# Kernel tuning notes

Hardware: AMD Instinct MI355X
Metric: run time of the kernel (lower is better)

## Reference

```python
import jax, jax.numpy as jnp
import numpy as np
from jax import lax


def setup_inputs() -> dict:
    key = jax.random.key(0)
    B, N, R = 16, 4096, 256
    param = jax.random.normal(key, (B, N, R), dtype=jnp.float32)
    return {"param": param}


def reference(param) -> jnp.ndarray:
    # StiefelHouseholder.forward with is_thin=True (rank != n):
    #   v = tril(param, -1) + eye(n, rank)      -> unit-lower columns v_i
    #   tau_i = 2 / ||v_i||^2
    #   Q = (I - tau_1 v_1 v_1^T) ... (I - tau_R v_R v_R^T) @ I[:, :R]
    B, N, R = param.shape
    eye = jnp.eye(N, R, dtype=param.dtype)                      # [N, R]
    v = jnp.tril(param, k=-1) + eye[None]                       # [B, N, R]
    tau = 2.0 / jnp.sum(v * v, axis=1)                          # [B, R]

    Q0 = jnp.broadcast_to(eye, (B, N, R))                       # start from thin identity

    def body(Q, i):
        vi = v[:, :, i]                                          # [B, N]
        ti = tau[:, i]                                           # [B]
        w = jnp.einsum('bn,bnk->bk', vi, Q)                      # v_i^T Q
        Q = Q - (ti[:, None] * vi)[:, :, None] * w[:, None, :]   # rank-1 update
        return Q, None

    # Apply H_R first (rightmost factor), then H_{R-1}, ..., H_1.
    Q, _ = lax.scan(body, Q0, jnp.arange(R - 1, -1, -1))
    return Q                                                     # thin [B, N, R]
```

## Files before the change

kernel.cpp:

```cpp
#include <hip/hip_runtime.h>
#include <stdint.h>

#define B_ 16
#define N_ 4096
#define R_ 256

typedef short bf16x8 __attribute__((ext_vector_type(8)));
typedef float f32x4 __attribute__((ext_vector_type(4)));
typedef uint32_t u32;


__device__ __forceinline__ u32 pack_split(float x) {
  u32 u = __float_as_uint(x);
  u32 h = u & 0xffff0000u;
  float l = x - __uint_as_float(h);
  return h | (__float_as_uint(l) >> 16);
}

__device__ __forceinline__ void unpack8(const u32* w, bf16x8& hi, bf16x8& lo) {
  union { u32 u[4]; bf16x8 v; } H, L;
#pragma unroll
  for (int i = 0; i < 4; ++i) {
    u32 a = w[2 * i], b = w[2 * i + 1];
    H.u[i] = (a >> 16) | (b & 0xffff0000u);
    L.u[i] = (a & 0xffffu) | (b << 16);
  }
  hi = H.v; lo = L.v;
}

__device__ __forceinline__ void read_frag(const u32* rowbase, int row, int q2,
                                          bf16x8& hi, bf16x8& lo) {
  u32 w[8];
  const int s = row & 7;
  *(uint4*)&w[0] = *(const uint4*)(rowbase + (((q2    ) ^ s) << 2));
  *(uint4*)&w[4] = *(const uint4*)(rowbase + (((q2 + 1) ^ s) << 2));
  unpack8(w, hi, lo);
}

__device__ __forceinline__ f32x4 mm3(bf16x8 ah, bf16x8 al, bf16x8 bh, bf16x8 bl,
                                     f32x4 c) {
  c = __builtin_amdgcn_mfma_f32_16x16x32_bf16(al, bh, c, 0, 0, 0);
  c = __builtin_amdgcn_mfma_f32_16x16x32_bf16(ah, bl, c, 0, 0, 0);
  c = __builtin_amdgcn_mfma_f32_16x16x32_bf16(ah, bh, c, 0, 0, 0);
  return c;
}

__global__ __launch_bounds__(256) void gram_kernel(const float* __restrict__ param,
                                                   float* __restrict__ SP) {
  const int tile = blockIdx.x, chunk = blockIdx.y, b = blockIdx.z;
  const int j0 = (tile == 2) ? 128 : 0;
  const int k0 = (tile == 0) ? 0 : 128;
  const float* __restrict__ P = param + (size_t)b * N_ * R_;

  __shared__ u32 VT[256][32];

  const int t = threadIdx.x;
  const int lane = t & 63, wv = t >> 6;
  const int wr = wv >> 1, wc = wv & 1;
  const int l15 = lane & 15, q = lane >> 4;
  const int bbase = (tile == 1) ? 128 : 0;

  f32x4 acc[4][4];
#pragma unroll
  for (int i = 0; i < 4; ++i)
#pragma unroll
    for (int j = 0; j < 4; ++j) acc[i][j] = (f32x4){0.f, 0.f, 0.f, 0.f};

  const int nb = chunk * 256;
  const int ns = (nb > k0) ? nb : k0;
  const int ne = nb + 256;

  float ld[32];

  const int ct1 = t;
  const int ct0 = t & 127;
  const int gc0 = j0 + ct0;
  const int hb  = t >> 7;

  auto do_load = [&](int n0) {
    if (tile == 1) {
#pragma unroll
      for (int ri = 0; ri < 8; ++ri)
#pragma unroll
        for (int s = 0; s < 4; ++s)
          ld[4 * ri + s] = P[(size_t)(n0 + 4 * ri + s) * R_ + ct1];
    } else {
#pragma unroll
      for (int ri = 0; ri < 4; ++ri)
#pragma unroll
        for (int s = 0; s < 4; ++s)
          ld[4 * ri + s] = P[(size_t)(n0 + 4 * (2 * ri + hb) + s) * R_ + gc0];
    }
  };

  auto do_write = [&](int n0) {
    if (tile == 1) {
#pragma unroll
      for (int ri = 0; ri < 8; ++ri) {
        u32 qw[4];
#pragma unroll
        for (int s = 0; s < 4; ++s) {
          int n = n0 + 4 * ri + s;
          float v = (n == ct1) ? 1.f : ((n > ct1) ? ld[4 * ri + s] : 0.f);
          qw[s] = pack_split(v);
        }
        *(uint4*)&VT[ct1][((ri ^ (ct1 & 7)) << 2)] = *(uint4*)qw;
      }
    } else {
#pragma unroll
      for (int ri = 0; ri < 4; ++ri) {
        int ch = 2 * ri + hb;
        u32 qw[4];
#pragma unroll
        for (int s = 0; s < 4; ++s) {
          int n = n0 + 4 * ch + s;
          float v = (n == gc0) ? 1.f : ((n > gc0) ? ld[4 * ri + s] : 0.f);
          qw[s] = pack_split(v);
        }
        *(uint4*)&VT[ct0][((ch ^ (ct0 & 7)) << 2)] = *(uint4*)qw;
      }
    }
  };

  do_load(ns);
  for (int n0 = ns; n0 < ne; n0 += 32) {
    do_write(n0);
    __syncthreads();
    if (n0 + 32 < ne) do_load(n0 + 32);

    bf16x8 Ah[4], Al[4];
#pragma unroll
    for (int mt = 0; mt < 4; ++mt) {
      int row = 64 * wr + 16 * mt + l15;
      read_frag(&VT[row][0], row, 2 * q, Ah[mt], Al[mt]);
    }
#pragma unroll
    for (int nt = 0; nt < 4; ++nt) {
      int brow = bbase + 64 * wc + 16 * nt + l15;
      bf16x8 bh, bl;
      read_frag(&VT[brow][0], brow, 2 * q, bh, bl);
#pragma unroll
      for (int mt = 0; mt < 4; ++mt)
        acc[mt][nt] = mm3(Ah[mt], Al[mt], bh, bl, acc[mt][nt]);
    }
    __syncthreads();
  }

  float* Sp = SP + (size_t)(chunk * 16 + b) * (R_ * R_);
#pragma unroll
  for (int mt = 0; mt < 4; ++mt)
#pragma unroll
    for (int nt = 0; nt < 4; ++nt) {
      int jj = j0 + 64 * wr + 16 * mt + 4 * q;
      int kk = k0 + 64 * wc + 16 * nt + l15;
#pragma unroll
      for (int r = 0; r < 4; ++r)
        Sp[(size_t)(jj + r) * R_ + kk] = acc[mt][nt][r];
    }
}

__global__ __launch_bounds__(256) void reduce_kernel(float* __restrict__ SP) {
  size_t idx = (size_t)blockIdx.x * 256 + threadIdx.x;
  float4* sp = (float4*)SP;
  float4 a = sp[idx];
#pragma unroll
  for (int c = 1; c < 16; ++c) {
    float4 v = sp[idx + (size_t)c * 262144];
    a.x += v.x; a.y += v.y; a.z += v.z; a.w += v.w;
  }
  sp[idx] = a;
}

#define DPP_ADD(v, ctrl, rmask)                                              \
  v += __int_as_float(__builtin_amdgcn_update_dpp(                           \
      0, __float_as_int(v), ctrl, rmask, 0xf, true))

__global__ __launch_bounds__(1024) void solve_kernel(const float* __restrict__ param,
                                                     const float* __restrict__ S,
                                                     u32* __restrict__ WtP) {
  extern __shared__ float tri[];
  const int t    = threadIdx.x;
  const int lane = t & 63;
  const int wave = t >> 6;
  const int b    = blockIdx.x >> 4;
  const int jg   = blockIdx.x & 15;
  const int k    = jg + 16 * wave;
  const float* __restrict__ Sb = S + (size_t)b * R_ * R_;
  const float* __restrict__ Pb = param + (size_t)b * N_ * R_;

  float4 x = *(const float4*)(Pb + (size_t)k * R_ + 4 * lane);
  {
    int c0 = 4 * lane;
    x.x = (c0     == k) ? 1.f : ((c0     < k) ? x.x : 0.f);
    x.y = (c0 + 1 == k) ? 1.f : ((c0 + 1 < k) ? x.y : 0.f);
    x.z = (c0 + 2 == k) ? 1.f : ((c0 + 2 < k) ? x.z : 0.f);
    x.w = (c0 + 3 == k) ? 1.f : ((c0 + 3 < k) ? x.w : 0.f);
  }

  const float4* S4 = (const float4*)Sb;
#pragma unroll
  for (int m = 0; m < 16; ++m) {
    int idx = t + 1024 * m;
    int r  = idx >> 6;
    int c4 = idx & 63;
    int g  = r >> 2;
    if (c4 >= g) {
      float4 v = S4[idx];
      int rowlen = 256 - 4 * g;
      int addr = 1024 * g - 8 * g * (g - 1) + (r & 3) * rowlen + 4 * (c4 - g);
      *(float4*)&tri[addr] = v;
    }
  }
  __syncthreads();

  float4 w = make_float4(0.f, 0.f, 0.f, 0.f);
  const int k4 = k >> 2;
  int rowlen = 256 - 4 * k4;
  int base   = 1024 * k4 - 8 * k4 * (k4 - 1);

  for (int r4 = k4;; --r4) {
    const float* rb = tri + base + 4 * lane - 4 * r4;
    float4 rA0 = *(const float4*)(rb);
    float4 rA1 = *(const float4*)(rb + rowlen);
    float4 rA2 = *(const float4*)(rb + 2 * rowlen);
    float4 rA3 = *(const float4*)(rb + 3 * rowlen);

    float s0 = fmaf(rA0.x, w.x, fmaf(rA0.y, w.y, fmaf(rA0.z, w.z, rA0.w * w.w)));
    float s1 = fmaf(rA1.x, w.x, fmaf(rA1.y, w.y, fmaf(rA1.z, w.z, rA1.w * w.w)));
    float s2 = fmaf(rA2.x, w.x, fmaf(rA2.y, w.y, fmaf(rA2.z, w.z, rA2.w * w.w)));
    float s3 = fmaf(rA3.x, w.x, fmaf(rA3.y, w.y, fmaf(rA3.z, w.z, rA3.w * w.w)));

    DPP_ADD(s0, 0x111, 0xf); DPP_ADD(s1, 0x111, 0xf);
    DPP_ADD(s2, 0x111, 0xf); DPP_ADD(s3, 0x111, 0xf);
    DPP_ADD(s0, 0x112, 0xf); DPP_ADD(s1, 0x112, 0xf);
    DPP_ADD(s2, 0x112, 0xf); DPP_ADD(s3, 0x112, 0xf);
    DPP_ADD(s0, 0x114, 0xf); DPP_ADD(s1, 0x114, 0xf);
    DPP_ADD(s2, 0x114, 0xf); DPP_ADD(s3, 0x114, 0xf);
    DPP_ADD(s0, 0x118, 0xf); DPP_ADD(s1, 0x118, 0xf);
    DPP_ADD(s2, 0x118, 0xf); DPP_ADD(s3, 0x118, 0xf);
    DPP_ADD(s0, 0x142, 0xa); DPP_ADD(s1, 0x142, 0xa);
    DPP_ADD(s2, 0x142, 0xa); DPP_ADD(s3, 0x142, 0xa);
    DPP_ADD(s0, 0x143, 0xc); DPP_ADD(s1, 0x143, 0xc);
    DPP_ADD(s2, 0x143, 0xc); DPP_ADD(s3, 0x143, 0xc);
    s0 = __int_as_float(__builtin_amdgcn_readlane(__float_as_int(s0), 63));
    s1 = __int_as_float(__builtin_amdgcn_readlane(__float_as_int(s1), 63));
    s2 = __int_as_float(__builtin_amdgcn_readlane(__float_as_int(s2), 63));
    s3 = __int_as_float(__builtin_amdgcn_readlane(__float_as_int(s3), 63));

    float w3 = 2.f * __builtin_amdgcn_rcpf(rA3.w) * (x.w - s3);
    float s2c = fmaf(rA2.w, w3, s2);
    float w2 = 2.f * __builtin_amdgcn_rcpf(rA2.z) * (x.z - s2c);
    float s1c = fmaf(rA1.z, w2, fmaf(rA1.w, w3, s1));
    float w1 = 2.f * __builtin_amdgcn_rcpf(rA1.y) * (x.y - s1c);
    float s0c = fmaf(rA0.y, w1, fmaf(rA0.z, w2, fmaf(rA0.w, w3, s0)));
    float w0 = 2.f * __builtin_amdgcn_rcpf(rA0.x) * (x.x - s0c);
    if (lane == r4) { w.w = w3; w.z = w2; w.y = w1; w.x = w0; }

    if (r4 == 0) break;
    rowlen += 4;
    base   -= 4 * rowlen;
  }

  u32 pw[4] = { pack_split(w.x), pack_split(w.y), pack_split(w.z), pack_split(w.w) };
  *(uint4*)(WtP + ((size_t)b * R_ + k) * R_ + 4 * lane) = *(uint4*)pw;
}

__global__ __launch_bounds__(256) void final_kernel(const float* __restrict__ param,
                                                    const u32* __restrict__ WtP,
                                                    float* __restrict__ Q) {
  const int b  = blockIdx.z;
  const int n0 = blockIdx.x * 128;
  const int k0 = blockIdx.y * 128;
  const float* __restrict__ Pb = param + (size_t)b * N_ * R_;
  const u32* __restrict__ Wb = WtP + (size_t)b * R_ * R_;
  float* __restrict__ Qb = Q + (size_t)b * N_ * R_;

  __shared__ u32 VA[128][32];
  __shared__ u32 WB[128][32];

  const int t = threadIdx.x;
  const int lane = t & 63, wv = t >> 6;
  const int wr = wv >> 1, wc = wv & 1;
  const int l15 = lane & 15, q = lane >> 4;
  const int row8 = t >> 3;
  const int c4 = t & 7;

  f32x4 acc[4][4];
#pragma unroll
  for (int i = 0; i < 4; ++i)
#pragma unroll
    for (int j = 0; j < 4; ++j) acc[i][j] = (f32x4){0.f, 0.f, 0.f, 0.f};

  const int jend = k0 + 128;
  for (int jb = 0; jb < jend; jb += 32) {
#pragma unroll
    for (int pi = 0; pi < 4; ++pi) {
      int row = row8 + 32 * pi;
      int n = n0 + row;
      int gj = jb + 4 * c4;
      float4 v = *(const float4*)&Pb[(size_t)n * R_ + gj];
      u32 qw[4];
      qw[0] = pack_split((n == gj    ) ? 1.f : ((n > gj    ) ? v.x : 0.f));
      qw[1] = pack_split((n == gj + 1) ? 1.f : ((n > gj + 1) ? v.y : 0.f));
      qw[2] = pack_split((n == gj + 2) ? 1.f : ((n > gj + 2) ? v.z : 0.f));
      qw[3] = pack_split((n == gj + 3) ? 1.f : ((n > gj + 3) ? v.w : 0.f));
      *(uint4*)&VA[row][((c4 ^ (row & 7)) << 2)] = *(uint4*)qw;
      uint4 wq = *(const uint4*)&Wb[(size_t)(k0 + row) * R_ + gj];
      *(uint4*)&WB[row][((c4 ^ (row & 7)) << 2)] = wq;
    }
    __syncthreads();

    bf16x8 Ah[4], Al[4];
#pragma unroll
    for (int mt = 0; mt < 4; ++mt) {
      int row = 64 * wr + 16 * mt + l15;
      read_frag(&VA[row][0], row, 2 * q, Ah[mt], Al[mt]);
    }
#pragma unroll
    for (int nt = 0; nt < 4; ++nt) {
      int krow = 64 * wc + 16 * nt + l15;
      bf16x8 bh, bl;
      read_frag(&WB[krow][0], krow, 2 * q, bh, bl);
#pragma unroll
      for (int mt = 0; mt < 4; ++mt)
        acc[mt][nt] = mm3(Ah[mt], Al[mt], bh, bl, acc[mt][nt]);
    }
    __syncthreads();
  }

#pragma unroll
  for (int mt = 0; mt < 4; ++mt)
#pragma unroll
    for (int nt = 0; nt < 4; ++nt) {
      int nrow = n0 + 64 * wr + 16 * mt + 4 * q;
      int kcol = k0 + 64 * wc + 16 * nt + l15;
#pragma unroll
      for (int r = 0; r < 4; ++r) {
        float val = ((nrow + r == kcol) ? 1.f : 0.f) - acc[mt][nt][r];
        Qb[(size_t)(nrow + r) * R_ + kcol] = val;
      }
    }
}

extern "C" void kernel_launch(void* const* d_in, const int* in_sizes, int n_in,
                              void* d_out, int out_size, void* d_ws, size_t ws_size,
                              hipStream_t stream) {
  const float* param = (const float*)d_in[0];
  float* Q  = (float*)d_out;
  float* SP = Q;
  float* S  = Q;
  u32*   WtP = (u32*)d_ws;

  gram_kernel<<<dim3(3, 16, B_), 256, 0, stream>>>(param, SP);
  reduce_kernel<<<dim3(1024), 256, 0, stream>>>(SP);
  solve_kernel<<<dim3(256), 1024, 133120, stream>>>(param, S, WtP);
  final_kernel<<<dim3(32, 2, B_), 256, 0, stream>>>(param, WtP, Q);
}
```

Before: 149.3 us.

## Async global-to-LDS loads and LDS-staged coalesced stores in final kernel

The final kernel now loads the param and W tiles with global_load_lds async copies, issuing the next tile before the MFMA work so loads overlap compute. The raw float V tile is stored in LDS and split into bf16 hi/lo at fragment read time, with the triangular mask applied only to the diagonal blocks. The epilogue stages results through LDS so the Q output is written as coalesced float4 rows instead of scattered scalar stores. The cost is extra barriers and more split work per fragment read, and the epilogue reuses VAf (128x32 floats) with a row stride of 132 for 32 rows, which looks like it overruns the array.

```diff
diff --git a/kernel.cpp b/kernel.cpp
--- a/kernel.cpp
+++ b/kernel.cpp
@@ -37,12 +37,38 @@
   unpack8(w, hi, lo);
 }
 
+__device__ __forceinline__ void read_frag_f(const float* rowbase, int row, int q2,
+                                            bf16x8& hi, bf16x8& lo) {
+  float w[8];
+  const int s = row & 7;
+  *(float4*)&w[0] = *(const float4*)(rowbase + (((q2    ) ^ s) << 2));
+  *(float4*)&w[4] = *(const float4*)(rowbase + (((q2 + 1) ^ s) << 2));
+  union { u32 u[4]; bf16x8 v; } H, L;
+#pragma unroll
+  for (int i = 0; i < 4; ++i) {
+    u32 a = __float_as_uint(w[2 * i]);
+    u32 b = __float_as_uint(w[2 * i + 1]);
+    u32 ah = a & 0xffff0000u, bh = b & 0xffff0000u;
+    float la = w[2 * i]     - __uint_as_float(ah);
+    float lb = w[2 * i + 1] - __uint_as_float(bh);
+    H.u[i] = (a >> 16) | bh;
+    L.u[i] = (__float_as_uint(la) >> 16) | (__float_as_uint(lb) & 0xffff0000u);
+  }
+  hi = H.v; lo = L.v;
+}
+
 __device__ __forceinline__ f32x4 mm3(bf16x8 ah, bf16x8 al, bf16x8 bh, bf16x8 bl,
                                      f32x4 c) {
   c = __builtin_amdgcn_mfma_f32_16x16x32_bf16(al, bh, c, 0, 0, 0);
   c = __builtin_amdgcn_mfma_f32_16x16x32_bf16(ah, bl, c, 0, 0, 0);
   c = __builtin_amdgcn_mfma_f32_16x16x32_bf16(ah, bh, c, 0, 0, 0);
   return c;
+}
+
+typedef __attribute__((address_space(1))) const u32* gas_p;
+typedef __attribute__((address_space(3))) u32* las_p;
+__device__ __forceinline__ void async_cp16(void* lds, const void* g) {
+  __builtin_amdgcn_global_load_lds((gas_p)g, (las_p)lds, 16, 0, 0);
 }
 
 __global__ __launch_bounds__(256) void gram_kernel(const float* __restrict__ param,
@@ -275,15 +301,16 @@
   const u32* __restrict__ Wb = WtP + (size_t)b * R_ * R_;
   float* __restrict__ Qb = Q + (size_t)b * N_ * R_;
 
-  __shared__ u32 VA[128][32];
-  __shared__ u32 WB[128][32];
+  __shared__ float VAf[128][32];
+  __shared__ u32   WBp[128][32];
 
   const int t = threadIdx.x;
   const int lane = t & 63, wv = t >> 6;
   const int wr = wv >> 1, wc = wv & 1;
   const int l15 = lane & 15, q = lane >> 4;
-  const int row8 = t >> 3;
-  const int c4 = t & 7;
+  const int rsub = lane >> 3;
+  const int csub = lane & 7;
+  const int chsw = csub ^ rsub;
 
   f32x4 acc[4][4];
 #pragma unroll
@@ -291,55 +318,82 @@
 #pragma unroll
     for (int j = 0; j < 4; ++j) acc[i][j] = (f32x4){0.f, 0.f, 0.f, 0.f};
 
+  auto issue = [&](int jb) {
+#pragma unroll
+    for (int c = 0; c < 4; ++c) {
+      int rbase = 32 * c + 8 * wv;
+      int row   = rbase + rsub;
+      async_cp16(&VAf[rbase][0], &Pb[(size_t)(n0 + row) * R_ + jb + 4 * chsw]);
+      async_cp16(&WBp[rbase][0], &Wb[(size_t)(k0 + row) * R_ + jb + 4 * chsw]);
+    }
+  };
+
   const int jend = k0 + 128;
+  issue(0);
   for (int jb = 0; jb < jend; jb += 32) {
-#pragma unroll
-    for (int pi = 0; pi < 4; ++pi) {
-      int row = row8 + 32 * pi;
-      int n = n0 + row;
-      int gj = jb + 4 * c4;
-      float4 v = *(const float4*)&Pb[(size_t)n * R_ + gj];
-      u32 qw[4];
-      qw[0] = pack_split((n == gj    ) ? 1.f : ((n > gj    ) ? v.x : 0.f));
-      qw[1] = pack_split((n == gj + 1) ? 1.f : ((n > gj + 1) ? v.y : 0.f));
-      qw[2] = pack_split((n == gj + 2) ? 1.f : ((n > gj + 2) ? v.z : 0.f));
-      qw[3] = pack_split((n == gj + 3) ? 1.f : ((n > gj + 3) ? v.w : 0.f));
-      *(uint4*)&VA[row][((c4 ^ (row & 7)) << 2)] = *(uint4*)qw;
-      uint4 wq = *(const uint4*)&Wb[(size_t)(k0 + row) * R_ + gj];
-      *(uint4*)&WB[row][((c4 ^ (row & 7)) << 2)] = wq;
-    }
-    __syncthreads();
-
-    bf16x8 Ah[4], Al[4];
+    __syncthreads();
+
+    if (n0 < 256 && n0 <= jb + 31) {
+#pragma unroll
+      for (int m = 0; m < 16; ++m) {
+        int idx = t + 256 * m;
+        int row = idx >> 5;
+        int j   = idx & 31;
+        int n   = n0 + row;
+        int gj  = jb + j;
+        if (n <= gj)
+          VAf[row][(((j >> 2) ^ (row & 7)) << 2) + (j & 3)] = (n == gj) ? 1.f : 0.f;
+      }
+      __syncthreads();
+    }
+
+    bf16x8 Ah[4], Al[4], Bh[4], Bl[4];
 #pragma unroll
     for (int mt = 0; mt < 4; ++mt) {
       int row = 64 * wr + 16 * mt + l15;
-      read_frag(&VA[row][0], row, 2 * q, Ah[mt], Al[mt]);
+      read_frag_f(&VAf[row][0], row, 2 * q, Ah[mt], Al[mt]);
     }
 #pragma unroll
     for (int nt = 0; nt < 4; ++nt) {
       int krow = 64 * wc + 16 * nt + l15;
-      bf16x8 bh, bl;
-      read_frag(&WB[krow][0], krow, 2 * q, bh, bl);
+      read_frag(&WBp[krow][0], krow, 2 * q, Bh[nt], Bl[nt]);
+    }
+    __syncthreads();
+
+    if (jb + 32 < jend) issue(jb + 32);
+
+#pragma unroll
+    for (int nt = 0; nt < 4; ++nt)
 #pragma unroll
       for (int mt = 0; mt < 4; ++mt)
-        acc[mt][nt] = mm3(Ah[mt], Al[mt], bh, bl, acc[mt][nt]);
-    }
-    __syncthreads();
-  }
-
-#pragma unroll
-  for (int mt = 0; mt < 4; ++mt)
+        acc[mt][nt] = mm3(Ah[mt], Al[mt], Bh[nt], Bl[nt], acc[mt][nt]);
+  }
+
+  float* Ep = (float*)&VAf[0][0];
+  const int erow = t >> 3;
+  const int ec16 = (t & 7) * 16;
+#pragma unroll
+  for (int mt = 0; mt < 4; ++mt) {
+    __syncthreads();
 #pragma unroll
     for (int nt = 0; nt < 4; ++nt) {
-      int nrow = n0 + 64 * wr + 16 * mt + 4 * q;
       int kcol = k0 + 64 * wc + 16 * nt + l15;
 #pragma unroll
       for (int r = 0; r < 4; ++r) {
-        float val = ((nrow + r == kcol) ? 1.f : 0.f) - acc[mt][nt][r];
-        Qb[(size_t)(nrow + r) * R_ + kcol] = val;
+        int nrow = n0 + 64 * wr + 16 * mt + 4 * q + r;
+        int lrow = 16 * wr + 4 * q + r;
+        Ep[lrow * 132 + 64 * wc + 16 * nt + l15] =
+            ((nrow == kcol) ? 1.f : 0.f) - acc[mt][nt][r];
       }
     }
+    __syncthreads();
+    int grow = n0 + 64 * (erow >> 4) + 16 * mt + (erow & 15);
+#pragma unroll
+    for (int s = 0; s < 4; ++s) {
+      float4 v = *(const float4*)&Ep[erow * 132 + ec16 + 4 * s];
+      *(float4*)&Qb[(size_t)grow * R_ + k0 + ec16 + 4 * s] = v;
+    }
+  }
 }
 
 extern "C" void kernel_launch(void* const* d_in, const int* in_sizes, int n_in,
```

After: 138.8 us. 1.08x faster.
